# Kernel optimization log

Measured on AMD Instinct MI355X. Metric: run time of the kernel, lower is better.

## Reference

```python
import jax, jax.numpy as jnp
import numpy as np

N = 262144
H = 256
R = 32


def setup_inputs() -> dict:
    key = jax.random.key(0)
    ks = jax.random.split(key, 16)
    s = 1.0 / np.sqrt(H)
    return {
        "x": jax.random.normal(ks[0], (N, 1), jnp.float32),
        "t": jax.random.uniform(ks[1], (N, 1), jnp.float32),
        "start_w": jax.random.normal(ks[2], (H, 2), jnp.float32) * 0.5,
        "start_b": jax.random.normal(ks[3], (H,), jnp.float32) * 0.1,
        "end_w": jax.random.normal(ks[4], (1, H), jnp.float32) * s,
        "end_b": jax.random.normal(ks[5], (1,), jnp.float32) * 0.1,
        "col_0": jax.random.normal(ks[6], (H, R), jnp.float32) * s,
        "col_1": jax.random.normal(ks[7], (H, R), jnp.float32) * s,
        "col_2": jax.random.normal(ks[8], (H, R), jnp.float32) * s,
        "row_0": jax.random.normal(ks[9], (H, R), jnp.float32) * s,
        "row_1": jax.random.normal(ks[10], (H, R), jnp.float32) * s,
        "row_2": jax.random.normal(ks[11], (H, R), jnp.float32) * s,
        "alpha_0": jax.random.normal(ks[12], (R,), jnp.float32),
        "alpha_1": jax.random.normal(ks[13], (R,), jnp.float32),
        "alpha_2": jax.random.normal(ks[14], (R,), jnp.float32),
    }


def reference(x, t, start_w, start_b, end_w, end_b,
              col_0, col_1, col_2, row_0, row_1, row_2,
              alpha_0, alpha_1, alpha_2):
    # inputs: [N,2] -> start Linear -> tanh
    inp = jnp.concatenate([x, t], axis=1)
    h = jnp.tanh(inp @ start_w.T + start_b)  # [N, H]
    # three low-rank blocks: h @ (col * diag(alpha)) @ row.T, then tanh.
    # col_basis @ diag(alpha) == col_basis * alpha[None, :] (column scaling)
    for col, row, alpha in ((col_0, row_0, alpha_0),
                            (col_1, row_1, alpha_1),
                            (col_2, row_2, alpha_2)):
        h = jnp.tanh((h @ (col * alpha)) @ row.T)  # [N,H]->[N,R]->[N,H]
    return h @ end_w.T + end_b  # [N, 1]
```

## Files before the change

### kernel.cpp

```cpp
#include <hip/hip_runtime.h>


typedef _Float16 half4_t __attribute__((ext_vector_type(4)));
typedef _Float16 half2_t __attribute__((ext_vector_type(2)));
typedef __fp16   fp16x2  __attribute__((ext_vector_type(2)));
typedef float    float4_t __attribute__((ext_vector_type(4)));

#define TANH_SCALE 2.885390081777927f
#define MFMA16 __builtin_amdgcn_mfma_f32_16x16x16f16

namespace {

struct alignas(16) Smem {
  half4_t ctf[3 * 16 * 2 * 64];
  half4_t rwf[3 * 16 * 2 * 64];
  float w0[256], w1[256], bb[256];
  float ew[256];
};

__device__ __forceinline__ half4_t pack4(float4_t v) {
  union { fp16x2 f2[2]; half4_t h4; } u;
  u.f2[0] = __builtin_amdgcn_cvt_pkrtz(v.x, v.y);
  u.f2[1] = __builtin_amdgcn_cvt_pkrtz(v.z, v.w);
  return u.h4;
}

__device__ __forceinline__ float tanh_pre(float y) {
  const float e = __builtin_amdgcn_exp2f(y);
  return fmaf(-2.0f, __builtin_amdgcn_rcpf(e + 1.0f), 1.0f);
}

__device__ __forceinline__ half4_t tanh4(float4_t v) {
  float4_t r;
  r.x = tanh_pre(v.x); r.y = tanh_pre(v.y);
  r.z = tanh_pre(v.z); r.w = tanh_pre(v.w);
  return pack4(r);
}

__global__ __launch_bounds__(1024)
__attribute__((amdgpu_waves_per_eu(4, 4)))
void pinn_fused(
    const float* __restrict__ xg, const float* __restrict__ tg,
    const float* __restrict__ sw, const float* __restrict__ sb,
    const float* __restrict__ ewp, const float* __restrict__ ebp,
    const float* __restrict__ c0, const float* __restrict__ c1,
    const float* __restrict__ c2, const float* __restrict__ r0,
    const float* __restrict__ r1, const float* __restrict__ r2,
    const float* __restrict__ a0, const float* __restrict__ a1,
    const float* __restrict__ a2, float* __restrict__ out, int n)
{
  __shared__ Smem sm;
  const int tid = threadIdx.x;

  for (int e = tid; e < 3 * 16 * 2 * 64; e += 1024) {
    const int lane_ = e & 63;
    const int sel   = (e >> 6) & 1;
    const int t_    = (e >> 7) & 15;
    const int k_    = e >> 11;
    const int m_ = lane_ & 15, q_ = lane_ >> 4;
    const float* ck = (k_ == 0) ? c0 : (k_ == 1) ? c1 : c2;
    const float* rk = (k_ == 0) ? r0 : (k_ == 1) ? r1 : r2;
    const float* ak = (k_ == 0) ? a0 : (k_ == 1) ? a1 : a2;
    {
      const int r = sel * 16 + m_;
      const float av = ak[r];
      const int j0 = 16 * t_ + 4 * q_;
      half4_t v;
      v.x = (_Float16)(ck[(j0 + 0) * 32 + r] * av);
      v.y = (_Float16)(ck[(j0 + 1) * 32 + r] * av);
      v.z = (_Float16)(ck[(j0 + 2) * 32 + r] * av);
      v.w = (_Float16)(ck[(j0 + 3) * 32 + r] * av);
      sm.ctf[e] = v;
    }
    {
      const int j = 16 * t_ + m_;
      const int rr = sel * 16 + 4 * q_;
      half4_t v;
      v.x = (_Float16)(rk[j * 32 + rr + 0] * TANH_SCALE);
      v.y = (_Float16)(rk[j * 32 + rr + 1] * TANH_SCALE);
      v.z = (_Float16)(rk[j * 32 + rr + 2] * TANH_SCALE);
      v.w = (_Float16)(rk[j * 32 + rr + 3] * TANH_SCALE);
      sm.rwf[e] = v;
    }
  }
  if (tid < 256) {
    sm.w0[tid] = sw[2 * tid] * TANH_SCALE;
    sm.w1[tid] = sw[2 * tid + 1] * TANH_SCALE;
    sm.bb[tid] = sb[tid] * TANH_SCALE;
    sm.ew[tid] = ewp[tid];
  }
  __syncthreads();

  const int wave = tid >> 6;
  const int lane = tid & 63;
  const int m = lane & 15;
  const int q = lane >> 4;
  const int wo = 4 * q;
  const float ebv = ebp[0];
  const int tiles = n >> 4;

  const float4_t z4 = {0.f, 0.f, 0.f, 0.f};

#pragma unroll 1
  for (int g = blockIdx.x * 32 + wave * 2; g < tiles; g += 8192) {
    const int n0 = g * 16;
    const int n1 = n0 + 16;
    const float xm0 = xg[n0 + m], tm0 = tg[n0 + m];
    const float xm1 = xg[n1 + m], tm1 = tg[n1 + m];

    float4_t a00 = z4, a01 = z4, a10 = z4, a11 = z4;
    float4_t zc0, zc1;
    {
      const float4_t w0v = *(const float4_t*)&sm.w0[wo];
      const float4_t w1v = *(const float4_t*)&sm.w1[wo];
      const float4_t bv  = *(const float4_t*)&sm.bb[wo];
      zc0.x = fmaf(xm0, w0v.x, fmaf(tm0, w1v.x, bv.x));
      zc1.x = fmaf(xm1, w0v.x, fmaf(tm1, w1v.x, bv.x));
      zc0.y = fmaf(xm0, w0v.y, fmaf(tm0, w1v.y, bv.y));
      zc1.y = fmaf(xm1, w0v.y, fmaf(tm1, w1v.y, bv.y));
      zc0.z = fmaf(xm0, w0v.z, fmaf(tm0, w1v.z, bv.z));
      zc1.z = fmaf(xm1, w0v.z, fmaf(tm1, w1v.z, bv.z));
      zc0.w = fmaf(xm0, w0v.w, fmaf(tm0, w1v.w, bv.w));
      zc1.w = fmaf(xm1, w0v.w, fmaf(tm1, w1v.w, bv.w));
    }
    const half4_t* cp0 = &sm.ctf[lane];
#pragma unroll 1
    for (int t = 0; t < 15; ++t) {
      const int cb = (t + 1) * 16 + wo;
      const float4_t w0v = *(const float4_t*)&sm.w0[cb];
      const float4_t w1v = *(const float4_t*)&sm.w1[cb];
      const float4_t bv  = *(const float4_t*)&sm.bb[cb];
      const half4_t h0 = tanh4(zc0);
      const half4_t h1 = tanh4(zc1);
      float4_t zn0, zn1;
      zn0.x = fmaf(xm0, w0v.x, fmaf(tm0, w1v.x, bv.x));
      zn1.x = fmaf(xm1, w0v.x, fmaf(tm1, w1v.x, bv.x));
      zn0.y = fmaf(xm0, w0v.y, fmaf(tm0, w1v.y, bv.y));
      zn1.y = fmaf(xm1, w0v.y, fmaf(tm1, w1v.y, bv.y));
      zn0.z = fmaf(xm0, w0v.z, fmaf(tm0, w1v.z, bv.z));
      zn1.z = fmaf(xm1, w0v.z, fmaf(tm1, w1v.z, bv.z));
      zn0.w = fmaf(xm0, w0v.w, fmaf(tm0, w1v.w, bv.w));
      zn1.w = fmaf(xm1, w0v.w, fmaf(tm1, w1v.w, bv.w));
      const half4_t cA = cp0[0], cB = cp0[64];
      a00 = MFMA16(cA, h0, a00, 0, 0, 0);
      a10 = MFMA16(cA, h1, a10, 0, 0, 0);
      a01 = MFMA16(cB, h0, a01, 0, 0, 0);
      a11 = MFMA16(cB, h1, a11, 0, 0, 0);
      zc0 = zn0; zc1 = zn1;
      cp0 += 128;
    }
    {
      const half4_t h0 = tanh4(zc0);
      const half4_t h1 = tanh4(zc1);
      const half4_t cA = cp0[0], cB = cp0[64];
      a00 = MFMA16(cA, h0, a00, 0, 0, 0);
      a10 = MFMA16(cA, h1, a10, 0, 0, 0);
      a01 = MFMA16(cB, h0, a01, 0, 0, 0);
      a11 = MFMA16(cB, h1, a11, 0, 0, 0);
    }

#pragma unroll 1
    for (int k = 0; k < 2; ++k) {
      const half4_t pA0 = pack4(a00), pB0 = pack4(a01);
      const half4_t pA1 = pack4(a10), pB1 = pack4(a11);
      const half4_t* rp = &sm.rwf[k * 2048 + lane];
      const half4_t* cp = &sm.ctf[(k + 1) * 2048 + lane];
      float4_t hc0, hc1;
      {
        const half4_t rA = rp[0], rB = rp[64];
        hc0 = MFMA16(rA, pA0, z4, 0, 0, 0);
        hc1 = MFMA16(rA, pA1, z4, 0, 0, 0);
        hc0 = MFMA16(rB, pB0, hc0, 0, 0, 0);
        hc1 = MFMA16(rB, pB1, hc1, 0, 0, 0);
      }
      float4_t n00 = z4, n01 = z4, n10 = z4, n11 = z4;
#pragma unroll 1
      for (int t = 0; t < 15; ++t) {
        const half4_t rA = rp[128], rB = rp[192];
        const half4_t cA = cp[0],  cB = cp[64];
        const half4_t h0 = tanh4(hc0);
        const half4_t h1 = tanh4(hc1);
        float4_t u0 = MFMA16(rA, pA0, z4, 0, 0, 0);
        float4_t u1 = MFMA16(rA, pA1, z4, 0, 0, 0);
        u0 = MFMA16(rB, pB0, u0, 0, 0, 0);
        u1 = MFMA16(rB, pB1, u1, 0, 0, 0);
        n00 = MFMA16(cA, h0, n00, 0, 0, 0);
        n10 = MFMA16(cA, h1, n10, 0, 0, 0);
        n01 = MFMA16(cB, h0, n01, 0, 0, 0);
        n11 = MFMA16(cB, h1, n11, 0, 0, 0);
        hc0 = u0; hc1 = u1;
        rp += 128; cp += 128;
      }
      {
        const half4_t cA = cp[0], cB = cp[64];
        const half4_t h0 = tanh4(hc0);
        const half4_t h1 = tanh4(hc1);
        n00 = MFMA16(cA, h0, n00, 0, 0, 0);
        n10 = MFMA16(cA, h1, n10, 0, 0, 0);
        n01 = MFMA16(cB, h0, n01, 0, 0, 0);
        n11 = MFMA16(cB, h1, n11, 0, 0, 0);
      }
      a00 = n00; a01 = n01; a10 = n10; a11 = n11;
    }

    float ssum0 = 0.0f, ssum1 = 0.0f;
    {
      const half4_t pA0 = pack4(a00), pB0 = pack4(a01);
      const half4_t pA1 = pack4(a10), pB1 = pack4(a11);
      const half4_t* rp = &sm.rwf[2 * 2048 + lane];
      float4_t hc0, hc1;
      {
        const half4_t rA = rp[0], rB = rp[64];
        hc0 = MFMA16(rA, pA0, z4, 0, 0, 0);
        hc1 = MFMA16(rA, pA1, z4, 0, 0, 0);
        hc0 = MFMA16(rB, pB0, hc0, 0, 0, 0);
        hc1 = MFMA16(rB, pB1, hc1, 0, 0, 0);
      }
#pragma unroll 1
      for (int t = 0; t < 15; ++t) {
        const half4_t rA = rp[128], rB = rp[192];
        const float4_t ev = *(const float4_t*)&sm.ew[t * 16 + wo];
        float4_t u0 = MFMA16(rA, pA0, z4, 0, 0, 0);
        float4_t u1 = MFMA16(rA, pA1, z4, 0, 0, 0);
        u0 = MFMA16(rB, pB0, u0, 0, 0, 0);
        u1 = MFMA16(rB, pB1, u1, 0, 0, 0);
        ssum0 = fmaf(ev.x, tanh_pre(hc0.x), ssum0);
        ssum1 = fmaf(ev.x, tanh_pre(hc1.x), ssum1);
        ssum0 = fmaf(ev.y, tanh_pre(hc0.y), ssum0);
        ssum1 = fmaf(ev.y, tanh_pre(hc1.y), ssum1);
        ssum0 = fmaf(ev.z, tanh_pre(hc0.z), ssum0);
        ssum1 = fmaf(ev.z, tanh_pre(hc1.z), ssum1);
        ssum0 = fmaf(ev.w, tanh_pre(hc0.w), ssum0);
        ssum1 = fmaf(ev.w, tanh_pre(hc1.w), ssum1);
        hc0 = u0; hc1 = u1;
        rp += 128;
      }
      {
        const float4_t ev = *(const float4_t*)&sm.ew[240 + wo];
        ssum0 = fmaf(ev.x, tanh_pre(hc0.x), ssum0);
        ssum1 = fmaf(ev.x, tanh_pre(hc1.x), ssum1);
        ssum0 = fmaf(ev.y, tanh_pre(hc0.y), ssum0);
        ssum1 = fmaf(ev.y, tanh_pre(hc1.y), ssum1);
        ssum0 = fmaf(ev.z, tanh_pre(hc0.z), ssum0);
        ssum1 = fmaf(ev.z, tanh_pre(hc1.z), ssum1);
        ssum0 = fmaf(ev.w, tanh_pre(hc0.w), ssum0);
        ssum1 = fmaf(ev.w, tanh_pre(hc1.w), ssum1);
      }
    }

    ssum0 += __shfl_xor(ssum0, 16);
    ssum0 += __shfl_xor(ssum0, 32);
    ssum1 += __shfl_xor(ssum1, 16);
    ssum1 += __shfl_xor(ssum1, 32);
    if (lane < 16) {
      out[n0 + m] = ssum0 + ebv;
      out[n1 + m] = ssum1 + ebv;
    }
  }
}

}

extern "C" void kernel_launch(void* const* d_in, const int* in_sizes, int n_in,
                              void* d_out, int out_size, void* d_ws, size_t ws_size,
                              hipStream_t stream) {
  const float* xg  = (const float*)d_in[0];
  const float* tg  = (const float*)d_in[1];
  const float* sw  = (const float*)d_in[2];
  const float* sb  = (const float*)d_in[3];
  const float* ewp = (const float*)d_in[4];
  const float* ebp = (const float*)d_in[5];
  const float* c0  = (const float*)d_in[6];
  const float* c1  = (const float*)d_in[7];
  const float* c2  = (const float*)d_in[8];
  const float* r0  = (const float*)d_in[9];
  const float* r1  = (const float*)d_in[10];
  const float* r2  = (const float*)d_in[11];
  const float* a0  = (const float*)d_in[12];
  const float* a1  = (const float*)d_in[13];
  const float* a2  = (const float*)d_in[14];
  float* outp = (float*)d_out;

  const int n = in_sizes[0];

  pinn_fused<<<256, 1024, 0, stream>>>(xg, tg, sw, sb, ewp, ebp,
                                       c0, c1, c2, r0, r1, r2, a0, a1, a2,
                                       outp, n);
}
```

Baseline: 150.1 us.

## Move row fragments to global workspace and double occupancy per CU

```diff
diff --git a/kernel.cpp b/kernel.cpp
--- a/kernel.cpp
+++ b/kernel.cpp
@@ -2,18 +2,17 @@
 
 
 typedef _Float16 half4_t __attribute__((ext_vector_type(4)));
-typedef _Float16 half2_t __attribute__((ext_vector_type(2)));
 typedef __fp16   fp16x2  __attribute__((ext_vector_type(2)));
 typedef float    float4_t __attribute__((ext_vector_type(4)));
 
 #define TANH_SCALE 2.885390081777927f
 #define MFMA16 __builtin_amdgcn_mfma_f32_16x16x16f16
+#define NFRAG (3 * 16 * 2 * 64)
 
 namespace {
 
 struct alignas(16) Smem {
-  half4_t ctf[3 * 16 * 2 * 64];
-  half4_t rwf[3 * 16 * 2 * 64];
+  half4_t ctf[NFRAG];
   float w0[256], w1[256], bb[256];
   float ew[256];
 };
@@ -37,51 +36,59 @@
   return pack4(r);
 }
 
+__global__ __launch_bounds__(1024) void stage_rwf(
+    const float* __restrict__ r0, const float* __restrict__ r1,
+    const float* __restrict__ r2, half4_t* __restrict__ ws)
+{
+  const int e = blockIdx.x * 1024 + threadIdx.x;
+  if (e >= NFRAG) return;
+  const int lane_ = e & 63;
+  const int sel   = (e >> 6) & 1;
+  const int t_    = (e >> 7) & 15;
+  const int k_    = e >> 11;
+  const int m_ = lane_ & 15, q_ = lane_ >> 4;
+  const float* rk = (k_ == 0) ? r0 : (k_ == 1) ? r1 : r2;
+  const int j = 16 * t_ + m_;
+  const int rr = sel * 16 + 4 * q_;
+  half4_t v;
+  v.x = (_Float16)(rk[j * 32 + rr + 0] * TANH_SCALE);
+  v.y = (_Float16)(rk[j * 32 + rr + 1] * TANH_SCALE);
+  v.z = (_Float16)(rk[j * 32 + rr + 2] * TANH_SCALE);
+  v.w = (_Float16)(rk[j * 32 + rr + 3] * TANH_SCALE);
+  ws[e] = v;
+}
+
 __global__ __launch_bounds__(1024)
-__attribute__((amdgpu_waves_per_eu(4, 4)))
+__attribute__((amdgpu_waves_per_eu(8, 8)))
 void pinn_fused(
     const float* __restrict__ xg, const float* __restrict__ tg,
     const float* __restrict__ sw, const float* __restrict__ sb,
     const float* __restrict__ ewp, const float* __restrict__ ebp,
     const float* __restrict__ c0, const float* __restrict__ c1,
-    const float* __restrict__ c2, const float* __restrict__ r0,
-    const float* __restrict__ r1, const float* __restrict__ r2,
-    const float* __restrict__ a0, const float* __restrict__ a1,
-    const float* __restrict__ a2, float* __restrict__ out, int n)
+    const float* __restrict__ c2, const float* __restrict__ a0,
+    const float* __restrict__ a1, const float* __restrict__ a2,
+    const half4_t* __restrict__ rwg, float* __restrict__ out, int n)
 {
   __shared__ Smem sm;
   const int tid = threadIdx.x;
 
-  for (int e = tid; e < 3 * 16 * 2 * 64; e += 1024) {
+  for (int e = tid; e < NFRAG; e += 1024) {
     const int lane_ = e & 63;
     const int sel   = (e >> 6) & 1;
     const int t_    = (e >> 7) & 15;
     const int k_    = e >> 11;
     const int m_ = lane_ & 15, q_ = lane_ >> 4;
     const float* ck = (k_ == 0) ? c0 : (k_ == 1) ? c1 : c2;
-    const float* rk = (k_ == 0) ? r0 : (k_ == 1) ? r1 : r2;
     const float* ak = (k_ == 0) ? a0 : (k_ == 1) ? a1 : a2;
-    {
-      const int r = sel * 16 + m_;
-      const float av = ak[r];
-      const int j0 = 16 * t_ + 4 * q_;
-      half4_t v;
-      v.x = (_Float16)(ck[(j0 + 0) * 32 + r] * av);
-      v.y = (_Float16)(ck[(j0 + 1) * 32 + r] * av);
-      v.z = (_Float16)(ck[(j0 + 2) * 32 + r] * av);
-      v.w = (_Float16)(ck[(j0 + 3) * 32 + r] * av);
-      sm.ctf[e] = v;
-    }
-    {
-      const int j = 16 * t_ + m_;
-      const int rr = sel * 16 + 4 * q_;
-      half4_t v;
-      v.x = (_Float16)(rk[j * 32 + rr + 0] * TANH_SCALE);
-      v.y = (_Float16)(rk[j * 32 + rr + 1] * TANH_SCALE);
-      v.z = (_Float16)(rk[j * 32 + rr + 2] * TANH_SCALE);
-      v.w = (_Float16)(rk[j * 32 + rr + 3] * TANH_SCALE);
-      sm.rwf[e] = v;
-    }
+    const int r = sel * 16 + m_;
+    const float av = ak[r];
+    const int j0 = 16 * t_ + 4 * q_;
+    half4_t v;
+    v.x = (_Float16)(ck[(j0 + 0) * 32 + r] * av);
+    v.y = (_Float16)(ck[(j0 + 1) * 32 + r] * av);
+    v.z = (_Float16)(ck[(j0 + 2) * 32 + r] * av);
+    v.w = (_Float16)(ck[(j0 + 3) * 32 + r] * av);
+    sm.ctf[e] = v;
   }
   if (tid < 256) {
     sm.w0[tid] = sw[2 * tid] * TANH_SCALE;
@@ -102,103 +109,61 @@
   const float4_t z4 = {0.f, 0.f, 0.f, 0.f};
 
 #pragma unroll 1
-  for (int g = blockIdx.x * 32 + wave * 2; g < tiles; g += 8192) {
+  for (int g = (blockIdx.x * 16 + wave) * 2; g < tiles; g += 16384) {
     const int n0 = g * 16;
     const int n1 = n0 + 16;
     const float xm0 = xg[n0 + m], tm0 = tg[n0 + m];
     const float xm1 = xg[n1 + m], tm1 = tg[n1 + m];
 
     float4_t a00 = z4, a01 = z4, a10 = z4, a11 = z4;
-    float4_t zc0, zc1;
-    {
-      const float4_t w0v = *(const float4_t*)&sm.w0[wo];
-      const float4_t w1v = *(const float4_t*)&sm.w1[wo];
-      const float4_t bv  = *(const float4_t*)&sm.bb[wo];
-      zc0.x = fmaf(xm0, w0v.x, fmaf(tm0, w1v.x, bv.x));
-      zc1.x = fmaf(xm1, w0v.x, fmaf(tm1, w1v.x, bv.x));
-      zc0.y = fmaf(xm0, w0v.y, fmaf(tm0, w1v.y, bv.y));
-      zc1.y = fmaf(xm1, w0v.y, fmaf(tm1, w1v.y, bv.y));
-      zc0.z = fmaf(xm0, w0v.z, fmaf(tm0, w1v.z, bv.z));
-      zc1.z = fmaf(xm1, w0v.z, fmaf(tm1, w1v.z, bv.z));
-      zc0.w = fmaf(xm0, w0v.w, fmaf(tm0, w1v.w, bv.w));
-      zc1.w = fmaf(xm1, w0v.w, fmaf(tm1, w1v.w, bv.w));
-    }
     const half4_t* cp0 = &sm.ctf[lane];
 #pragma unroll 1
-    for (int t = 0; t < 15; ++t) {
-      const int cb = (t + 1) * 16 + wo;
+    for (int t = 0; t < 16; ++t) {
+      const int cb = t * 16 + wo;
       const float4_t w0v = *(const float4_t*)&sm.w0[cb];
       const float4_t w1v = *(const float4_t*)&sm.w1[cb];
       const float4_t bv  = *(const float4_t*)&sm.bb[cb];
-      const half4_t h0 = tanh4(zc0);
-      const half4_t h1 = tanh4(zc1);
-      float4_t zn0, zn1;
-      zn0.x = fmaf(xm0, w0v.x, fmaf(tm0, w1v.x, bv.x));
-      zn1.x = fmaf(xm1, w0v.x, fmaf(tm1, w1v.x, bv.x));
-      zn0.y = fmaf(xm0, w0v.y, fmaf(tm0, w1v.y, bv.y));
-      zn1.y = fmaf(xm1, w0v.y, fmaf(tm1, w1v.y, bv.y));
-      zn0.z = fmaf(xm0, w0v.z, fmaf(tm0, w1v.z, bv.z));
-      zn1.z = fmaf(xm1, w0v.z, fmaf(tm1, w1v.z, bv.z));
-      zn0.w = fmaf(xm0, w0v.w, fmaf(tm0, w1v.w, bv.w));
-      zn1.w = fmaf(xm1, w0v.w, fmaf(tm1, w1v.w, bv.w));
+      float4_t z0, z1;
+      z0.x = fmaf(xm0, w0v.x, fmaf(tm0, w1v.x, bv.x));
+      z1.x = fmaf(xm1, w0v.x, fmaf(tm1, w1v.x, bv.x));
+      z0.y = fmaf(xm0, w0v.y, fmaf(tm0, w1v.y, bv.y));
+      z1.y = fmaf(xm1, w0v.y, fmaf(tm1, w1v.y, bv.y));
+      z0.z = fmaf(xm0, w0v.z, fmaf(tm0, w1v.z, bv.z));
+      z1.z = fmaf(xm1, w0v.z, fmaf(tm1, w1v.z, bv.z));
+      z0.w = fmaf(xm0, w0v.w, fmaf(tm0, w1v.w, bv.w));
+      z1.w = fmaf(xm1, w0v.w, fmaf(tm1, w1v.w, bv.w));
+      const half4_t h0 = tanh4(z0);
+      const half4_t h1 = tanh4(z1);
       const half4_t cA = cp0[0], cB = cp0[64];
       a00 = MFMA16(cA, h0, a00, 0, 0, 0);
       a10 = MFMA16(cA, h1, a10, 0, 0, 0);
       a01 = MFMA16(cB, h0, a01, 0, 0, 0);
       a11 = MFMA16(cB, h1, a11, 0, 0, 0);
-      zc0 = zn0; zc1 = zn1;
       cp0 += 128;
-    }
-    {
-      const half4_t h0 = tanh4(zc0);
-      const half4_t h1 = tanh4(zc1);
-      const half4_t cA = cp0[0], cB = cp0[64];
-      a00 = MFMA16(cA, h0, a00, 0, 0, 0);
-      a10 = MFMA16(cA, h1, a10, 0, 0, 0);
-      a01 = MFMA16(cB, h0, a01, 0, 0, 0);
-      a11 = MFMA16(cB, h1, a11, 0, 0, 0);
     }
 
 #pragma unroll 1
     for (int k = 0; k < 2; ++k) {
       const half4_t pA0 = pack4(a00), pB0 = pack4(a01);
       const half4_t pA1 = pack4(a10), pB1 = pack4(a11);
-      const half4_t* rp = &sm.rwf[k * 2048 + lane];
+      float4_t n00 = z4, n01 = z4, n10 = z4, n11 = z4;
+      const half4_t* rp = &rwg[k * 2048 + lane];
       const half4_t* cp = &sm.ctf[(k + 1) * 2048 + lane];
-      float4_t hc0, hc1;
-      {
+#pragma unroll 1
+      for (int t = 0; t < 16; ++t) {
         const half4_t rA = rp[0], rB = rp[64];
-        hc0 = MFMA16(rA, pA0, z4, 0, 0, 0);
-        hc1 = MFMA16(rA, pA1, z4, 0, 0, 0);
-        hc0 = MFMA16(rB, pB0, hc0, 0, 0, 0);
-        hc1 = MFMA16(rB, pB1, hc1, 0, 0, 0);
-      }
-      float4_t n00 = z4, n01 = z4, n10 = z4, n11 = z4;
-#pragma unroll 1
-      for (int t = 0; t < 15; ++t) {
-        const half4_t rA = rp[128], rB = rp[192];
-        const half4_t cA = cp[0],  cB = cp[64];
-        const half4_t h0 = tanh4(hc0);
-        const half4_t h1 = tanh4(hc1);
+        const half4_t cA = cp[0], cB = cp[64];
         float4_t u0 = MFMA16(rA, pA0, z4, 0, 0, 0);
         float4_t u1 = MFMA16(rA, pA1, z4, 0, 0, 0);
         u0 = MFMA16(rB, pB0, u0, 0, 0, 0);
         u1 = MFMA16(rB, pB1, u1, 0, 0, 0);
+        const half4_t h0 = tanh4(u0);
+        const half4_t h1 = tanh4(u1);
         n00 = MFMA16(cA, h0, n00, 0, 0, 0);
         n10 = MFMA16(cA, h1, n10, 0, 0, 0);
         n01 = MFMA16(cB, h0, n01, 0, 0, 0);
         n11 = MFMA16(cB, h1, n11, 0, 0, 0);
-        hc0 = u0; hc1 = u1;
         rp += 128; cp += 128;
-      }
-      {
-        const half4_t cA = cp[0], cB = cp[64];
-        const half4_t h0 = tanh4(hc0);
-        const half4_t h1 = tanh4(hc1);
-        n00 = MFMA16(cA, h0, n00, 0, 0, 0);
-        n10 = MFMA16(cA, h1, n10, 0, 0, 0);
-        n01 = MFMA16(cB, h0, n01, 0, 0, 0);
-        n11 = MFMA16(cB, h1, n11, 0, 0, 0);
       }
       a00 = n00; a01 = n01; a10 = n10; a11 = n11;
     }
@@ -207,44 +172,24 @@
     {
       const half4_t pA0 = pack4(a00), pB0 = pack4(a01);
       const half4_t pA1 = pack4(a10), pB1 = pack4(a11);
-      const half4_t* rp = &sm.rwf[2 * 2048 + lane];
-      float4_t hc0, hc1;
-      {
+      const half4_t* rp = &rwg[2 * 2048 + lane];
+#pragma unroll 1
+      for (int t = 0; t < 16; ++t) {
         const half4_t rA = rp[0], rB = rp[64];
-        hc0 = MFMA16(rA, pA0, z4, 0, 0, 0);
-        hc1 = MFMA16(rA, pA1, z4, 0, 0, 0);
-        hc0 = MFMA16(rB, pB0, hc0, 0, 0, 0);
-        hc1 = MFMA16(rB, pB1, hc1, 0, 0, 0);
-      }
-#pragma unroll 1
-      for (int t = 0; t < 15; ++t) {
-        const half4_t rA = rp[128], rB = rp[192];
         const float4_t ev = *(const float4_t*)&sm.ew[t * 16 + wo];
         float4_t u0 = MFMA16(rA, pA0, z4, 0, 0, 0);
         float4_t u1 = MFMA16(rA, pA1, z4, 0, 0, 0);
         u0 = MFMA16(rB, pB0, u0, 0, 0, 0);
         u1 = MFMA16(rB, pB1, u1, 0, 0, 0);
-        ssum0 = fmaf(ev.x, tanh_pre(hc0.x), ssum0);
-        ssum1 = fmaf(ev.x, tanh_pre(hc1.x), ssum1);
-        ssum0 = fmaf(ev.y, tanh_pre(hc0.y), ssum0);
-        ssum1 = fmaf(ev.y, tanh_pre(hc1.y), ssum1);
-        ssum0 = fmaf(ev.z, tanh_pre(hc0.z), ssum0);
-        ssum1 = fmaf(ev.z, tanh_pre(hc1.z), ssum1);
-        ssum0 = fmaf(ev.w, tanh_pre(hc0.w), ssum0);
-        ssum1 = fmaf(ev.w, tanh_pre(hc1.w), ssum1);
-        hc0 = u0; hc1 = u1;
+        ssum0 = fmaf(ev.x, tanh_pre(u0.x), ssum0);
+        ssum1 = fmaf(ev.x, tanh_pre(u1.x), ssum1);
+        ssum0 = fmaf(ev.y, tanh_pre(u0.y), ssum0);
+        ssum1 = fmaf(ev.y, tanh_pre(u1.y), ssum1);
+        ssum0 = fmaf(ev.z, tanh_pre(u0.z), ssum0);
+        ssum1 = fmaf(ev.z, tanh_pre(u1.z), ssum1);
+        ssum0 = fmaf(ev.w, tanh_pre(u0.w), ssum0);
+        ssum1 = fmaf(ev.w, tanh_pre(u1.w), ssum1);
         rp += 128;
-      }
-      {
-        const float4_t ev = *(const float4_t*)&sm.ew[240 + wo];
-        ssum0 = fmaf(ev.x, tanh_pre(hc0.x), ssum0);
-        ssum1 = fmaf(ev.x, tanh_pre(hc1.x), ssum1);
-        ssum0 = fmaf(ev.y, tanh_pre(hc0.y), ssum0);
-        ssum1 = fmaf(ev.y, tanh_pre(hc1.y), ssum1);
-        ssum0 = fmaf(ev.z, tanh_pre(hc0.z), ssum0);
-        ssum1 = fmaf(ev.z, tanh_pre(hc1.z), ssum1);
-        ssum0 = fmaf(ev.w, tanh_pre(hc0.w), ssum0);
-        ssum1 = fmaf(ev.w, tanh_pre(hc1.w), ssum1);
       }
     }
 
@@ -280,10 +225,13 @@
   const float* a1  = (const float*)d_in[13];
   const float* a2  = (const float*)d_in[14];
   float* outp = (float*)d_out;
+  half4_t* ws = (half4_t*)d_ws;
 
   const int n = in_sizes[0];
 
-  pinn_fused<<<256, 1024, 0, stream>>>(xg, tg, sw, sb, ewp, ebp,
-                                       c0, c1, c2, r0, r1, r2, a0, a1, a2,
-                                       outp, n);
-}
+  stage_rwf<<<(NFRAG + 1023) / 1024, 1024, 0, stream>>>(r0, r1, r2, ws);
+
+  pinn_fused<<<512, 1024, 0, stream>>>(xg, tg, sw, sb, ewp, ebp,
+                                       c0, c1, c2, a0, a1, a2,
+                                       ws, outp, n);
+}
```

After: 144.9 us. 3.5% less time.
